# Performance work log

Hardware: AMD Instinct MI355X
Metric: run time of the kernel (lower is better)

## Reference

```python
import jax, jax.numpy as jnp
import numpy as np

B, T, C = 4, 4096, 1024
DEGREE, EXPAND = 2, 2
H = EXPAND * C  # selector / inner dim = 2048


def setup_inputs() -> dict:
    key = jax.random.key(0)
    ks = jax.random.split(key, 4)
    sc = lambda d: 1.0 / np.sqrt(d)
    return {
        "x": jax.random.normal(ks[0], (B, T, C), jnp.float32),
        "W_sel": jax.random.normal(ks[1], (C, H), jnp.float32) * sc(C),
        "W_agg": jax.random.normal(ks[2], (C, DEGREE * H), jnp.float32) * sc(C),
        "W_out": jax.random.normal(ks[3], (H, C), jnp.float32) * sc(H),
        "sqk_q": jnp.ones((H,), jnp.float32),
        "sqk_k": jnp.ones((DEGREE * H,), jnp.float32),
    }


def reference(x, W_sel, W_agg, W_out, sqk_q, sqk_k):
    # Selector branch on queries (gated): B,T,H
    s = jax.nn.silu(jnp.einsum('btc,ch->bth', x, W_sel) * sqk_q)
    # Aggregator branch on context: B,T,DEGREE*H
    h = jnp.einsum('btc,cd->btd', x, W_agg) * sqk_k
    chunks = jnp.split(h, DEGREE, axis=-1)
    # Polynomial expansion: sum_{d=1..DEGREE} prod_{k<=d} chunk_k  -> B,T,H
    p = chunks[0]
    poly = p
    for c in chunks[1:]:
        p = p * c
        poly = poly + p
    # Causal masked mean: tril(ones(T,T)) @ poly / row-count == cumsum / arange.
    # Honors the causal structure without materializing the T x T mask.
    denom = jnp.arange(1, T + 1, dtype=poly.dtype)[None, :, None]
    agg = jnp.cumsum(poly, axis=1) / denom  # B,T,H causal running mean
    # Mix selected queries with aggregated polynomial state, project out.
    return jnp.einsum('bth,hc->btc', s * agg, W_out)
```

## Files before the change

### kernel.cpp

```cpp
#include <hip/hip_runtime.h>
#include <hip/hip_bf16.h>
#include <stdint.h>

#define BB 4
#define TT 4096
#define CC 1024
#define HH 2048
#define MM (BB*TT)
#define NCK 32
#define CKS 128

using short8 = __attribute__((ext_vector_type(8))) short;
using f32x4  = __attribute__((ext_vector_type(4))) float;

__device__ __forceinline__ unsigned short f2bf(float f) {
    union { float f; uint32_t u; } v; v.f = f;
    uint32_t r = v.u + 0x7fffu + ((v.u >> 16) & 1u);
    return (unsigned short)(r >> 16);
}
__device__ __forceinline__ float bf2f(unsigned short s) {
    union { uint32_t u; float f; } v; v.u = ((uint32_t)s) << 16;
    return v.f;
}
__device__ __forceinline__ float bf_lo(uint32_t u) {
    union { uint32_t u; float f; } v; v.u = u << 16; return v.f;
}
__device__ __forceinline__ float bf_hi(uint32_t u) {
    union { uint32_t u; float f; } v; v.u = u & 0xFFFF0000u; return v.f;
}
__device__ __forceinline__ uint32_t pack2bf(float lo, float hi) {
    return ((uint32_t)f2bf(lo)) | (((uint32_t)f2bf(hi)) << 16);
}

__global__ void conv_x_kernel(const float* __restrict__ x, unsigned short* __restrict__ xb, int n4) {
    int i = blockIdx.x * blockDim.x + threadIdx.x;
    if (i >= n4) return;
    float4 v = ((const float4*)x)[i];
    ushort4 o;
    o.x = f2bf(v.x); o.y = f2bf(v.y); o.z = f2bf(v.z); o.w = f2bf(v.w);
    ((ushort4*)xb)[i] = o;
}

__global__ void trans_direct_kernel(const float* __restrict__ in, unsigned short* __restrict__ out,
                                    const float* __restrict__ scale, int R, int Cin) {
    __shared__ float tile[32][33];
    int c0 = blockIdx.x * 32, k0 = blockIdx.y * 32;
    int tx = threadIdx.x;
    for (int i = threadIdx.y; i < 32; i += 8) {
        float s = scale ? scale[c0 + tx] : 1.f;
        tile[i][tx] = in[(size_t)(k0 + i) * Cin + c0 + tx] * s;
    }
    __syncthreads();
    for (int i = threadIdx.y; i < 32; i += 8)
        out[(size_t)(c0 + i) * R + k0 + tx] = f2bf(tile[tx][i]);
}

__global__ void trans_pair_kernel(const float* __restrict__ in, unsigned short* __restrict__ out,
                                  const float* __restrict__ scale) {
    __shared__ float tile[32][33];
    int q0 = blockIdx.x * 32, k0 = blockIdx.y * 32;
    int g = q0 >> 5;
    int tx = threadIdx.x;
    int c = (tx < 16) ? (g * 16 + tx) : (2048 + g * 16 + tx - 16);
    float s = scale[c];
    for (int i = threadIdx.y; i < 32; i += 8)
        tile[i][tx] = in[(size_t)(k0 + i) * 4096 + c] * s;
    __syncthreads();
    for (int i = threadIdx.y; i < 32; i += 8)
        out[(size_t)(q0 + i) * 1024 + k0 + tx] = f2bf(tile[tx][i]);
}

__global__ __launch_bounds__(256) void gemm_fused_kernel(
    const unsigned short* __restrict__ A,
    const unsigned short* __restrict__ Bt,
    unsigned short* __restrict__ Sout,
    unsigned short* __restrict__ Pout)
{
    __shared__ __align__(16) unsigned short As[128 * 32];
    __shared__ __align__(16) unsigned short Bs[128 * 32];

    const int mt = blockIdx.x / 48;
    const int nt = blockIdx.x % 48;
    const int m0 = mt << 7, n0 = nt << 7;

    const int tid  = threadIdx.x;
    const int lane = tid & 63;
    const int wave = tid >> 6;
    const int l15  = lane & 15;
    const int quad = lane >> 4;
    const int wm = (wave >> 1) * 64;
    const int wn = (wave & 1) * 64;

    f32x4 acc[4][4];
#pragma unroll
    for (int i = 0; i < 4; i++)
#pragma unroll
        for (int j = 0; j < 4; j++) acc[i][j] = {0.f, 0.f, 0.f, 0.f};

    for (int k0 = 0; k0 < 1024; k0 += 32) {
#pragma unroll
        for (int it = 0; it < 2; it++) {
            int c  = it * 256 + tid;
            int r  = c >> 2;
            int kq = (c & 3) * 8;
            const unsigned short* ga = A  + (size_t)(m0 + r) * 1024 + k0 + kq;
            const unsigned short* gb = Bt + (size_t)(n0 + r) * 1024 + k0 + kq;
            __builtin_amdgcn_global_load_lds(
                (const __attribute__((address_space(1))) void*)ga,
                (__attribute__((address_space(3))) void*)&As[c * 8], 16, 0, 0);
            __builtin_amdgcn_global_load_lds(
                (const __attribute__((address_space(1))) void*)gb,
                (__attribute__((address_space(3))) void*)&Bs[c * 8], 16, 0, 0);
        }
        __syncthreads();

        short8 af[4], bf[4];
#pragma unroll
        for (int i = 0; i < 4; i++)
            af[i] = *(const short8*)&As[(wm + i * 16 + l15) * 32 + quad * 8];
#pragma unroll
        for (int j = 0; j < 4; j++)
            bf[j] = *(const short8*)&Bs[(wn + j * 16 + l15) * 32 + quad * 8];
#pragma unroll
        for (int i = 0; i < 4; i++)
#pragma unroll
            for (int j = 0; j < 4; j++)
                acc[i][j] = __builtin_amdgcn_mfma_f32_16x16x32_bf16(af[i], bf[j], acc[i][j], 0, 0, 0);
        __syncthreads();
    }

    if (nt < 16) {
#pragma unroll
        for (int i = 0; i < 4; i++)
#pragma unroll
            for (int j = 0; j < 4; j++) {
                int col = n0 + wn + j * 16 + l15;
#pragma unroll
                for (int r = 0; r < 4; r++) {
                    int row = m0 + wm + i * 16 + quad * 4 + r;
                    float v = acc[i][j][r];
                    v = v / (1.f + __expf(-v));
                    Sout[(size_t)row * 2048 + col] = f2bf(v);
                }
            }
    } else {
        int pbase = ((n0 - 2048 + wn) >> 1);
#pragma unroll
        for (int i = 0; i < 4; i++)
#pragma unroll
            for (int j = 0; j < 4; j += 2) {
                int pcol = pbase + (j >> 1) * 16 + l15;
#pragma unroll
                for (int r = 0; r < 4; r++) {
                    int row = m0 + wm + i * 16 + quad * 4 + r;
                    float a1 = acc[i][j][r];
                    float a2 = acc[i][j + 1][r];
                    Pout[(size_t)row * 2048 + pcol] = f2bf(a1 * (1.f + a2));
                }
            }
    }
}

__global__ __launch_bounds__(256) void gemm_out_kernel(
    const unsigned short* __restrict__ A,
    const unsigned short* __restrict__ Bt,
    float* __restrict__ Cout)
{
    __shared__ __align__(16) unsigned short As[128 * 32];
    __shared__ __align__(16) unsigned short Bs[128 * 32];

    const int mt = blockIdx.x >> 3;
    const int nt = blockIdx.x & 7;
    const int m0 = mt << 7, n0 = nt << 7;

    const int tid  = threadIdx.x;
    const int lane = tid & 63;
    const int wave = tid >> 6;
    const int l15  = lane & 15;
    const int quad = lane >> 4;
    const int wm = (wave >> 1) * 64;
    const int wn = (wave & 1) * 64;

    f32x4 acc[4][4];
#pragma unroll
    for (int i = 0; i < 4; i++)
#pragma unroll
        for (int j = 0; j < 4; j++) acc[i][j] = {0.f, 0.f, 0.f, 0.f};

    for (int k0 = 0; k0 < 2048; k0 += 32) {
#pragma unroll
        for (int it = 0; it < 2; it++) {
            int c  = it * 256 + tid;
            int r  = c >> 2;
            int kq = (c & 3) * 8;
            const unsigned short* ga = A  + (size_t)(m0 + r) * 2048 + k0 + kq;
            const unsigned short* gb = Bt + (size_t)(n0 + r) * 2048 + k0 + kq;
            __builtin_amdgcn_global_load_lds(
                (const __attribute__((address_space(1))) void*)ga,
                (__attribute__((address_space(3))) void*)&As[c * 8], 16, 0, 0);
            __builtin_amdgcn_global_load_lds(
                (const __attribute__((address_space(1))) void*)gb,
                (__attribute__((address_space(3))) void*)&Bs[c * 8], 16, 0, 0);
        }
        __syncthreads();

        short8 af[4], bf[4];
#pragma unroll
        for (int i = 0; i < 4; i++)
            af[i] = *(const short8*)&As[(wm + i * 16 + l15) * 32 + quad * 8];
#pragma unroll
        for (int j = 0; j < 4; j++)
            bf[j] = *(const short8*)&Bs[(wn + j * 16 + l15) * 32 + quad * 8];
#pragma unroll
        for (int i = 0; i < 4; i++)
#pragma unroll
            for (int j = 0; j < 4; j++)
                acc[i][j] = __builtin_amdgcn_mfma_f32_16x16x32_bf16(af[i], bf[j], acc[i][j], 0, 0, 0);
        __syncthreads();
    }

#pragma unroll
    for (int i = 0; i < 4; i++)
#pragma unroll
        for (int j = 0; j < 4; j++) {
            int col = n0 + wn + j * 16 + l15;
#pragma unroll
            for (int r = 0; r < 4; r++) {
                int row = m0 + wm + i * 16 + quad * 4 + r;
                Cout[(size_t)row * 1024 + col] = acc[i][j][r];
            }
        }
}

__global__ void chunk_sum_kernel(const unsigned short* __restrict__ poly, float* __restrict__ part) {
    int seg = blockIdx.x & 3;
    int ck  = (blockIdx.x >> 2) & (NCK - 1);
    int b   = blockIdx.x >> 7;
    int cp  = seg * 256 + threadIdx.x;
    size_t base = ((size_t)b * TT + (size_t)ck * CKS) * 2048 + cp * 2;
    float s0 = 0.f, s1 = 0.f;
    for (int t = 0; t < CKS; t++) {
        uint32_t v = *(const uint32_t*)&poly[base + (size_t)t * 2048];
        s0 += bf_lo(v);
        s1 += bf_hi(v);
    }
    size_t po = ((size_t)b * NCK + ck) * 2048 + cp * 2;
    part[po] = s0;
    part[po + 1] = s1;
}

__global__ void chunk_scan_kernel(float* __restrict__ part) {
    int idx = blockIdx.x * blockDim.x + threadIdx.x;
    int b = idx >> 11, col = idx & 2047;
    float run = 0.f;
    for (int ck = 0; ck < NCK; ck++) {
        size_t off = ((size_t)b * NCK + ck) * 2048 + col;
        float v = part[off];
        part[off] = run;
        run += v;
    }
}

__global__ void finalize_kernel(unsigned short* __restrict__ poly, const unsigned short* __restrict__ s,
                                const float* __restrict__ part) {
    int seg = blockIdx.x & 3;
    int ck  = (blockIdx.x >> 2) & (NCK - 1);
    int b   = blockIdx.x >> 7;
    int cp  = seg * 256 + threadIdx.x;
    size_t po = ((size_t)b * NCK + ck) * 2048 + cp * 2;
    float run0 = part[po], run1 = part[po + 1];
    size_t base = ((size_t)b * TT + (size_t)ck * CKS) * 2048 + cp * 2;
    for (int t = 0; t < CKS; t++) {
        int tg = ck * CKS + t;
        size_t off = base + (size_t)t * 2048;
        uint32_t pv = *(const uint32_t*)&poly[off];
        run0 += bf_lo(pv);
        run1 += bf_hi(pv);
        float inv = 1.f / (float)(tg + 1);
        uint32_t sv = *(const uint32_t*)&s[off];
        float m0 = bf_lo(sv) * run0 * inv;
        float m1 = bf_hi(sv) * run1 * inv;
        *(uint32_t*)&poly[off] = pack2bf(m0, m1);
    }
}

extern "C" void kernel_launch(void* const* d_in, const int* in_sizes, int n_in,
                              void* d_out, int out_size, void* d_ws, size_t ws_size,
                              hipStream_t stream) {
    const float* x     = (const float*)d_in[0];
    const float* W_sel = (const float*)d_in[1];
    const float* W_agg = (const float*)d_in[2];
    const float* W_out = (const float*)d_in[3];
    const float* sqk_q = (const float*)d_in[4];
    const float* sqk_k = (const float*)d_in[5];
    float* out = (float*)d_out;

    char* ws = (char*)d_ws;
    unsigned short* xb    = (unsigned short*)(ws);
    unsigned short* wallT = (unsigned short*)(ws + 33554432ull);
    unsigned short* woutT = (unsigned short*)(ws + 46137344ull);
    unsigned short* s_b   = (unsigned short*)(ws + 50331648ull);
    unsigned short* poly  = (unsigned short*)(ws + 117440512ull);
    float*          part  = (float*)(ws + 184549376ull);

    dim3 tb(32, 8);
    conv_x_kernel<<<(MM * CC / 4 + 255) / 256, 256, 0, stream>>>(x, xb, MM * CC / 4);
    trans_direct_kernel<<<dim3(HH / 32, CC / 32), tb, 0, stream>>>(W_sel, wallT, sqk_q, CC, HH);
    trans_pair_kernel<<<dim3(4096 / 32, CC / 32), tb, 0, stream>>>(W_agg, wallT + 2048ull * 1024, sqk_k);
    trans_direct_kernel<<<dim3(CC / 32, HH / 32), tb, 0, stream>>>(W_out, woutT, nullptr, HH, CC);

    gemm_fused_kernel<<<(MM / 128) * 48, 256, 0, stream>>>(xb, wallT, s_b, poly);

    chunk_sum_kernel<<<BB * NCK * 4, 256, 0, stream>>>(poly, part);
    chunk_scan_kernel<<<(BB * HH) / 256, 256, 0, stream>>>(part);
    finalize_kernel<<<BB * NCK * 4, 256, 0, stream>>>(poly, s_b, part);

    gemm_out_kernel<<<(MM / 128) * (CC / 128), 256, 0, stream>>>(poly, woutT, out);
}
```

Measured before the change: 541.5 us.

## Fuse chunk sums into GEMM epilogue and use K=64 swizzled LDS tiles

Per-chunk column sums of the polynomial output are now accumulated inside the fused GEMM epilogue through LDS atomics and written to the partial buffer. This removes the separate chunk_sum kernel and its full re-read of poly. Both GEMMs also move from a K step of 32 to 64, with an XOR-swizzled LDS layout meant to avoid bank conflicts and halve the barrier count per K. In exchange LDS use doubles, and the sums are taken in fp32 before bf16 rounding, which differs slightly from summing the stored values.

```diff
diff --git a/kernel.cpp b/kernel.cpp
--- a/kernel.cpp
+++ b/kernel.cpp
@@ -17,10 +17,6 @@
     union { float f; uint32_t u; } v; v.f = f;
     uint32_t r = v.u + 0x7fffu + ((v.u >> 16) & 1u);
     return (unsigned short)(r >> 16);
-}
-__device__ __forceinline__ float bf2f(unsigned short s) {
-    union { uint32_t u; float f; } v; v.u = ((uint32_t)s) << 16;
-    return v.f;
 }
 __device__ __forceinline__ float bf_lo(uint32_t u) {
     union { uint32_t u; float f; } v; v.u = u << 16; return v.f;
@@ -74,10 +70,12 @@
     const unsigned short* __restrict__ A,
     const unsigned short* __restrict__ Bt,
     unsigned short* __restrict__ Sout,
-    unsigned short* __restrict__ Pout)
+    unsigned short* __restrict__ Pout,
+    float* __restrict__ part)
 {
-    __shared__ __align__(16) unsigned short As[128 * 32];
-    __shared__ __align__(16) unsigned short Bs[128 * 32];
+    __shared__ __align__(16) unsigned short As[128 * 64];
+    __shared__ __align__(16) unsigned short Bs[128 * 64];
+    __shared__ float psum[64];
 
     const int mt = blockIdx.x / 48;
     const int nt = blockIdx.x % 48;
@@ -97,14 +95,14 @@
 #pragma unroll
         for (int j = 0; j < 4; j++) acc[i][j] = {0.f, 0.f, 0.f, 0.f};
 
-    for (int k0 = 0; k0 < 1024; k0 += 32) {
-#pragma unroll
-        for (int it = 0; it < 2; it++) {
+    for (int k0 = 0; k0 < 1024; k0 += 64) {
+#pragma unroll
+        for (int it = 0; it < 4; it++) {
             int c  = it * 256 + tid;
-            int r  = c >> 2;
-            int kq = (c & 3) * 8;
-            const unsigned short* ga = A  + (size_t)(m0 + r) * 1024 + k0 + kq;
-            const unsigned short* gb = Bt + (size_t)(n0 + r) * 1024 + k0 + kq;
+            int r  = c >> 3;
+            int sl = (c & 7) ^ (r & 7);
+            const unsigned short* ga = A  + (size_t)(m0 + r) * 1024 + k0 + sl * 8;
+            const unsigned short* gb = Bt + (size_t)(n0 + r) * 1024 + k0 + sl * 8;
             __builtin_amdgcn_global_load_lds(
                 (const __attribute__((address_space(1))) void*)ga,
                 (__attribute__((address_space(3))) void*)&As[c * 8], 16, 0, 0);
@@ -114,18 +112,27 @@
         }
         __syncthreads();
 
-        short8 af[4], bf[4];
-#pragma unroll
-        for (int i = 0; i < 4; i++)
-            af[i] = *(const short8*)&As[(wm + i * 16 + l15) * 32 + quad * 8];
-#pragma unroll
-        for (int j = 0; j < 4; j++)
-            bf[j] = *(const short8*)&Bs[(wn + j * 16 + l15) * 32 + quad * 8];
-#pragma unroll
-        for (int i = 0; i < 4; i++)
-#pragma unroll
-            for (int j = 0; j < 4; j++)
-                acc[i][j] = __builtin_amdgcn_mfma_f32_16x16x32_bf16(af[i], bf[j], acc[i][j], 0, 0, 0);
+#pragma unroll
+        for (int ks = 0; ks < 2; ks++) {
+            short8 af[4], bf[4];
+#pragma unroll
+            for (int i = 0; i < 4; i++) {
+                int row = wm + i * 16 + l15;
+                int ph = (quad + ks * 4) ^ (row & 7);
+                af[i] = *(const short8*)&As[row * 64 + ph * 8];
+            }
+#pragma unroll
+            for (int j = 0; j < 4; j++) {
+                int row = wn + j * 16 + l15;
+                int ph = (quad + ks * 4) ^ (row & 7);
+                bf[j] = *(const short8*)&Bs[row * 64 + ph * 8];
+            }
+#pragma unroll
+            for (int i = 0; i < 4; i++)
+#pragma unroll
+                for (int j = 0; j < 4; j++)
+                    acc[i][j] = __builtin_amdgcn_mfma_f32_16x16x32_bf16(af[i], bf[j], acc[i][j], 0, 0, 0);
+        }
         __syncthreads();
     }
 
@@ -144,20 +151,32 @@
                 }
             }
     } else {
+        if (tid < 64) psum[tid] = 0.f;
+        __syncthreads();
         int pbase = ((n0 - 2048 + wn) >> 1);
-#pragma unroll
-        for (int i = 0; i < 4; i++)
+        float lsum0 = 0.f, lsum1 = 0.f;
+#pragma unroll
+        for (int i = 0; i < 4; i++) {
 #pragma unroll
             for (int j = 0; j < 4; j += 2) {
                 int pcol = pbase + (j >> 1) * 16 + l15;
 #pragma unroll
                 for (int r = 0; r < 4; r++) {
                     int row = m0 + wm + i * 16 + quad * 4 + r;
-                    float a1 = acc[i][j][r];
-                    float a2 = acc[i][j + 1][r];
-                    Pout[(size_t)row * 2048 + pcol] = f2bf(a1 * (1.f + a2));
+                    float pv = acc[i][j][r] * (1.f + acc[i][j + 1][r]);
+                    Pout[(size_t)row * 2048 + pcol] = f2bf(pv);
+                    if (j == 0) lsum0 += pv; else lsum1 += pv;
                 }
             }
+        }
+        int pcl = (wn >> 1) + l15;
+        atomicAdd(&psum[pcl], lsum0);
+        atomicAdd(&psum[pcl + 16], lsum1);
+        __syncthreads();
+        if (tid < 64) {
+            int b = m0 >> 12, ck = (m0 & 4095) >> 7;
+            part[((size_t)b * NCK + ck) * 2048 + ((n0 - 2048) >> 1) + tid] = psum[tid];
+        }
     }
 }
 
@@ -166,8 +185,8 @@
     const unsigned short* __restrict__ Bt,
     float* __restrict__ Cout)
 {
-    __shared__ __align__(16) unsigned short As[128 * 32];
-    __shared__ __align__(16) unsigned short Bs[128 * 32];
+    __shared__ __align__(16) unsigned short As[128 * 64];
+    __shared__ __align__(16) unsigned short Bs[128 * 64];
 
     const int mt = blockIdx.x >> 3;
     const int nt = blockIdx.x & 7;
@@ -187,14 +206,14 @@
 #pragma unroll
         for (int j = 0; j < 4; j++) acc[i][j] = {0.f, 0.f, 0.f, 0.f};
 
-    for (int k0 = 0; k0 < 2048; k0 += 32) {
-#pragma unroll
-        for (int it = 0; it < 2; it++) {
+    for (int k0 = 0; k0 < 2048; k0 += 64) {
+#pragma unroll
+        for (int it = 0; it < 4; it++) {
             int c  = it * 256 + tid;
-            int r  = c >> 2;
-            int kq = (c & 3) * 8;
-            const unsigned short* ga = A  + (size_t)(m0 + r) * 2048 + k0 + kq;
-            const unsigned short* gb = Bt + (size_t)(n0 + r) * 2048 + k0 + kq;
+            int r  = c >> 3;
+            int sl = (c & 7) ^ (r & 7);
+            const unsigned short* ga = A  + (size_t)(m0 + r) * 2048 + k0 + sl * 8;
+            const unsigned short* gb = Bt + (size_t)(n0 + r) * 2048 + k0 + sl * 8;
             __builtin_amdgcn_global_load_lds(
                 (const __attribute__((address_space(1))) void*)ga,
                 (__attribute__((address_space(3))) void*)&As[c * 8], 16, 0, 0);
@@ -204,18 +223,27 @@
         }
         __syncthreads();
 
-        short8 af[4], bf[4];
-#pragma unroll
-        for (int i = 0; i < 4; i++)
-            af[i] = *(const short8*)&As[(wm + i * 16 + l15) * 32 + quad * 8];
-#pragma unroll
-        for (int j = 0; j < 4; j++)
-            bf[j] = *(const short8*)&Bs[(wn + j * 16 + l15) * 32 + quad * 8];
-#pragma unroll
-        for (int i = 0; i < 4; i++)
-#pragma unroll
-            for (int j = 0; j < 4; j++)
-                acc[i][j] = __builtin_amdgcn_mfma_f32_16x16x32_bf16(af[i], bf[j], acc[i][j], 0, 0, 0);
+#pragma unroll
+        for (int ks = 0; ks < 2; ks++) {
+            short8 af[4], bf[4];
+#pragma unroll
+            for (int i = 0; i < 4; i++) {
+                int row = wm + i * 16 + l15;
+                int ph = (quad + ks * 4) ^ (row & 7);
+                af[i] = *(const short8*)&As[row * 64 + ph * 8];
+            }
+#pragma unroll
+            for (int j = 0; j < 4; j++) {
+                int row = wn + j * 16 + l15;
+                int ph = (quad + ks * 4) ^ (row & 7);
+                bf[j] = *(const short8*)&Bs[row * 64 + ph * 8];
+            }
+#pragma unroll
+            for (int i = 0; i < 4; i++)
+#pragma unroll
+                for (int j = 0; j < 4; j++)
+                    acc[i][j] = __builtin_amdgcn_mfma_f32_16x16x32_bf16(af[i], bf[j], acc[i][j], 0, 0, 0);
+        }
         __syncthreads();
     }
 
@@ -230,23 +258,6 @@
                 Cout[(size_t)row * 1024 + col] = acc[i][j][r];
             }
         }
-}
-
-__global__ void chunk_sum_kernel(const unsigned short* __restrict__ poly, float* __restrict__ part) {
-    int seg = blockIdx.x & 3;
-    int ck  = (blockIdx.x >> 2) & (NCK - 1);
-    int b   = blockIdx.x >> 7;
-    int cp  = seg * 256 + threadIdx.x;
-    size_t base = ((size_t)b * TT + (size_t)ck * CKS) * 2048 + cp * 2;
-    float s0 = 0.f, s1 = 0.f;
-    for (int t = 0; t < CKS; t++) {
-        uint32_t v = *(const uint32_t*)&poly[base + (size_t)t * 2048];
-        s0 += bf_lo(v);
-        s1 += bf_hi(v);
-    }
-    size_t po = ((size_t)b * NCK + ck) * 2048 + cp * 2;
-    part[po] = s0;
-    part[po + 1] = s1;
 }
 
 __global__ void chunk_scan_kernel(float* __restrict__ part) {
@@ -309,9 +320,8 @@
     trans_pair_kernel<<<dim3(4096 / 32, CC / 32), tb, 0, stream>>>(W_agg, wallT + 2048ull * 1024, sqk_k);
     trans_direct_kernel<<<dim3(CC / 32, HH / 32), tb, 0, stream>>>(W_out, woutT, nullptr, HH, CC);
 
-    gemm_fused_kernel<<<(MM / 128) * 48, 256, 0, stream>>>(xb, wallT, s_b, poly);
-
-    chunk_sum_kernel<<<BB * NCK * 4, 256, 0, stream>>>(poly, part);
+    gemm_fused_kernel<<<(MM / 128) * 48, 256, 0, stream>>>(xb, wallT, s_b, poly, part);
+
     chunk_scan_kernel<<<(BB * HH) / 256, 256, 0, stream>>>(part);
     finalize_kernel<<<BB * NCK * 4, 256, 0, stream>>>(poly, s_b, part);
 
```

Result: faster. 525.7 us (-2.9%).
